# Performance work log

Hardware: AMD Instinct MI355X
Metric: run time of the kernel (lower is better)

The kernel has to match this reference:

```python
import jax, jax.numpy as jnp
import numpy as np

DIM = 1024
HEADS = 16
DIM_HEAD = 64
INNER = HEADS * DIM_HEAD  # 1024
SCALE = DIM_HEAD ** -0.5


def layernorm(x, gamma, beta, eps=1e-5):
    mu = jnp.mean(x, axis=-1, keepdims=True)
    var = jnp.var(x, axis=-1, keepdims=True)
    return (x - mu) * jax.lax.rsqrt(var + eps) * gamma + beta


def setup_inputs() -> dict:
    key = jax.random.key(0)
    ks = jax.random.split(key, 6)
    x = jax.random.normal(ks[0], (2, 2048, DIM), dtype=jnp.float32)
    # params (stored [in, out]; torch Linear does x @ W.T with W [out, in])
    w_q = jax.random.normal(ks[1], (DIM, INNER), dtype=jnp.float32) * (DIM ** -0.5)
    w_kv = jax.random.normal(ks[2], (DIM, 2 * INNER), dtype=jnp.float32) * (DIM ** -0.5)
    w_out = jax.random.normal(ks[3], (INNER, DIM), dtype=jnp.float32) * (INNER ** -0.5)
    b_out = jnp.zeros((DIM,), dtype=jnp.float32)
    gamma = jnp.ones((DIM,), dtype=jnp.float32)
    beta = jnp.zeros((DIM,), dtype=jnp.float32)
    return {"x": x, "w_q": w_q, "w_kv": w_kv, "w_out": w_out, "b_out": b_out,
            "gamma": gamma, "beta": beta}


def reference(x, w_q, w_kv, w_out, b_out, gamma, beta):
    b, n, _ = x.shape
    xn = layernorm(x, gamma, beta)
    q = xn @ w_q                           # [b, n, inner]
    kv = xn @ w_kv                         # [b, n, 2*inner]
    k, v = jnp.split(kv, 2, axis=-1)
    def split_heads(t):
        return t.reshape(b, n, HEADS, DIM_HEAD).transpose(0, 2, 1, 3)  # b h n d
    q, k, v = split_heads(q), split_heads(k), split_heads(v)
    dots = jnp.einsum('bhid,bhjd->bhij', q, k) * SCALE   # [b, h, n, n]
    attn = jax.nn.softmax(dots, axis=-1)
    out = jnp.einsum('bhij,bhjd->bhid', attn, v)          # [b, h, n, d]
    out = out.transpose(0, 2, 1, 3).reshape(b, n, INNER)  # b n (h d)
    return out @ w_out + b_out
```

## Files before the change

kernel.cpp:

```cpp
#include <hip/hip_runtime.h>

typedef unsigned short u16;
typedef u16   u16x8 __attribute__((ext_vector_type(8)));
typedef __bf16 bf16x8 __attribute__((ext_vector_type(8)));
typedef float f32x4 __attribute__((ext_vector_type(4)));
typedef float f32x2 __attribute__((ext_vector_type(2)));
typedef _Float16 f16x4 __attribute__((ext_vector_type(4)));
typedef _Float16 f16x8 __attribute__((ext_vector_type(8)));
typedef unsigned u32x2 __attribute__((ext_vector_type(2)));

__device__ __forceinline__ u16 f2b(float f){ __bf16 h=(__bf16)f; return __builtin_bit_cast(u16,h); }

__device__ __forceinline__ f32x4 mfma16(u16x8 a, u16x8 b, f32x4 c){
  return __builtin_amdgcn_mfma_f32_16x16x32_bf16(
      __builtin_bit_cast(bf16x8,a), __builtin_bit_cast(bf16x8,b), c, 0,0,0);
}

__device__ __forceinline__ void gl2lds16(const u16* g, u16* l){
  __builtin_amdgcn_global_load_lds((const __attribute__((address_space(1))) void*)g,
                                   (__attribute__((address_space(3))) void*)l, 16, 0, 0);
}

__global__ __launch_bounds__(256) void ln_kernel(const float* __restrict__ x,
                                                 const float* __restrict__ gamma,
                                                 const float* __restrict__ beta,
                                                 u16* __restrict__ xn){
  const int row = blockIdx.x, t = threadIdx.x;
  const float4 v = ((const float4*)(x + (size_t)row*1024))[t];
  float s  = v.x+v.y+v.z+v.w;
  float sq = v.x*v.x+v.y*v.y+v.z*v.z+v.w*v.w;
  for (int m=1;m<64;m<<=1){ s += __shfl_xor(s,m); sq += __shfl_xor(sq,m); }
  __shared__ float red[8];
  const int w=t>>6, l=t&63;
  if(l==0){ red[w]=s; red[4+w]=sq; }
  __syncthreads();
  const float S  = red[0]+red[1]+red[2]+red[3];
  const float SQ = red[4]+red[5]+red[6]+red[7];
  const float mu = S*(1.f/1024.f);
  const float var= SQ*(1.f/1024.f)-mu*mu;
  const float rs = rsqrtf(var+1e-5f);
  const float4 g4=((const float4*)gamma)[t], b4=((const float4*)beta)[t];
  u16 o0=f2b((v.x-mu)*rs*g4.x+b4.x);
  u16 o1=f2b((v.y-mu)*rs*g4.y+b4.y);
  u16 o2=f2b((v.z-mu)*rs*g4.z+b4.z);
  u16 o3=f2b((v.w-mu)*rs*g4.w+b4.w);
  uint2 p; p.x=(unsigned)o0|((unsigned)o1<<16); p.y=(unsigned)o2|((unsigned)o3<<16);
  ((uint2*)(xn + (size_t)row*1024))[t]=p;
}

__global__ __launch_bounds__(256) void wtrans_all_kernel(const float* __restrict__ wq,
    const float* __restrict__ wkv, const float* __restrict__ wout,
    u16* __restrict__ wqkvt, u16* __restrict__ woutt){
  __shared__ float tile[64][65];
  const int bx=blockIdx.x, t=threadIdx.x;
  const float* in; u16* out; int C, cxx;
  if(bx<16){ in=wq;  out=wqkvt;           C=1024; cxx=bx; }
  else if(bx<48){ in=wkv; out=wqkvt+1024*1024; C=2048; cxx=bx-16; }
  else { in=wout; out=woutt;             C=1024; cxx=bx-48; }
  const int R=1024;
  const int c0=cxx*64, r0=blockIdx.y*64;
  {
    const int r=t>>2, cc=t&3;
    const float* gp = in + (size_t)(r0+r)*C + c0 + cc*16;
    #pragma unroll
    for(int i=0;i<4;i++){
      float4 f=((const float4*)gp)[i];
      tile[r][cc*16+i*4+0]=f.x; tile[r][cc*16+i*4+1]=f.y;
      tile[r][cc*16+i*4+2]=f.z; tile[r][cc*16+i*4+3]=f.w;
    }
  }
  __syncthreads();
  const int c=t>>2, rc=t&3;
  u16x8 a,b;
  #pragma unroll
  for(int i=0;i<8;i++) a[i]=f2b(tile[rc*16+i][c]);
  #pragma unroll
  for(int i=0;i<8;i++) b[i]=f2b(tile[rc*16+8+i][c]);
  u16* op = out + (size_t)(c0+c)*R + r0 + rc*16;
  *(u16x8*)op=a; *(u16x8*)(op+8)=b;
}

template<int MODE,int TM>
__global__ __launch_bounds__(256) void gemm_bt_kernel(const u16* __restrict__ A,
    const u16* __restrict__ Bt, u16* __restrict__ outQ, u16* __restrict__ outK,
    u16* __restrict__ outV, float* __restrict__ outF, const float* __restrict__ bias,
    float scale, int M, int N, int K){
  constexpr int MT = TM/32;
  __shared__ u16 As[TM*64];
  __shared__ u16 Bs[128*64];
  const int t=threadIdx.x, w=t>>6, l=t&63, qd=l>>4, ln=l&15;
  const int m0=blockIdx.y*TM, n0=blockIdx.x*128;
  const int wm=(w>>1)*(TM/2), wn=(w&1)*64;
  f32x4 acc[MT][4] = {};
  const int nK = K>>6;
  for(int kt=0; kt<nK; kt++){
    const int k0=kt*64;
    #pragma unroll
    for(int p=0;p<MT;p++){
      const int cid=p*256+t, r=cid>>3, pc=cid&7, g=pc^(r&7);
      gl2lds16(A + (size_t)(m0+r)*K + k0 + g*8, &As[(p*256 + (t&192))*8]);
    }
    #pragma unroll
    for(int p=0;p<4;p++){
      const int cid=p*256+t, r=cid>>3, pc=cid&7, g=pc^(r&7);
      gl2lds16(Bt + (size_t)(n0+r)*K + k0 + g*8, &Bs[(p*256 + (t&192))*8]);
    }
    __syncthreads();
    #pragma unroll
    for(int ks=0;ks<2;ks++){
      u16x8 af[MT], bf[4];
      #pragma unroll
      for(int mt=0;mt<MT;mt++){
        const int m=wm+mt*16+ln, kc=ks*4+qd, pcc=kc^(m&7);
        af[mt]=*(const u16x8*)&As[m*64 + pcc*8];
      }
      #pragma unroll
      for(int nt=0;nt<4;nt++){
        const int n=wn+nt*16+ln, kc=ks*4+qd, pcc=kc^(n&7);
        bf[nt]=*(const u16x8*)&Bs[n*64 + pcc*8];
      }
      #pragma unroll
      for(int mt=0;mt<MT;mt++)
        #pragma unroll
        for(int nt=0;nt<4;nt++)
          acc[mt][nt]=mfma16(af[mt],bf[nt],acc[mt][nt]);
    }
    __syncthreads();
  }
  if(MODE==1){
    #pragma unroll
    for(int mt=0;mt<MT;mt++)
      #pragma unroll
      for(int rr=0;rr<4;rr++){
        const int row = m0+wm+mt*16+qd*4+rr;
        #pragma unroll
        for(int nt=0;nt<4;nt++){
          const int col = n0+wn+nt*16+ln;
          outF[(size_t)row*N+col]=acc[mt][nt][rr]+bias[col];
        }
      }
  } else if(n0<1024){
    #pragma unroll
    for(int mt=0;mt<MT;mt++)
      #pragma unroll
      for(int rr=0;rr<4;rr++){
        const int row = m0+wm+mt*16+qd*4+rr;
        #pragma unroll
        for(int nt=0;nt<4;nt++)
          outQ[(size_t)row*1024 + n0+wn+nt*16+ln]=f2b(acc[mt][nt][rr]*scale);
      }
  } else if(n0<2048){
    u16* kp = outK + (size_t)((m0>>11)*16 + ((n0-1024+wn)>>6))*131072;
    const int jb = (m0&2047) + wm;
    #pragma unroll
    for(int mt=0;mt<MT;mt++)
      #pragma unroll
      for(int rr=0;rr<4;rr++){
        const int j = jb + mt*16 + qd*4 + rr;
        #pragma unroll
        for(int nt=0;nt<4;nt++)
          kp[(size_t)j*64 + nt*16+ln]=f2b(acc[mt][nt][rr]);
      }
  } else {
    u16* vpp = outV + (size_t)((m0>>11)*16 + ((n0-2048+wn)>>6))*131072;
    const int jb = (m0&2047) + wm;
    #pragma unroll
    for(int mt=0;mt<MT;mt++){
      const int j = jb + mt*16 + qd*4;
      const int vbase = ((j>>5)*4 + ((j>>2)&3))*512 + ((j>>4)&1)*4;
      #pragma unroll
      for(int nt=0;nt<4;nt++){
        const auto lo=__builtin_amdgcn_cvt_pkrtz(acc[mt][nt][0],acc[mt][nt][1]);
        const auto hi=__builtin_amdgcn_cvt_pkrtz(acc[mt][nt][2],acc[mt][nt][3]);
        uint2 w2; w2.x=__builtin_bit_cast(unsigned,lo); w2.y=__builtin_bit_cast(unsigned,hi);
        *(uint2*)&vpp[vbase + (nt*16+ln)*8] = w2;
      }
    }
  }
}

__global__ __launch_bounds__(256,4) void attn_kernel(const u16* __restrict__ Q,
    const u16* __restrict__ Kp, const u16* __restrict__ Vp, u16* __restrict__ O){
  __shared__ u16 Ks[8192];
  __shared__ u16 Vs[8192];
  const int qt=blockIdx.x, h=blockIdx.y, bb=blockIdx.z;
  const int t=threadIdx.x, w=t>>6, l=t&63, qd=l>>4, ln=l&15;
  const int q0=qt*64;
  const size_t baseQ=(size_t)bb*2048*1024 + h*64;
  const size_t baseKV=(size_t)(bb*16+h)*131072;
  u16x8 qf[2];
  #pragma unroll
  for(int ks=0;ks<2;ks++)
    qf[ks] = *(const u16x8*)(Q + baseQ + (size_t)(q0+w*16+ln)*1024 + ks*32+qd*8);
  f32x2 l2={0.f,0.f};
  f32x4 o_acc[4]={};
  const f32x4 zf={0.f,0.f,0.f,0.f};

  for(int j0=0;j0<2048;j0+=128){
    __syncthreads();
    #pragma unroll
    for(int p=0;p<4;p++){
      const int r=(p*256+t)>>3, g=(t&7)^((t>>3)&7);
      gl2lds16(Kp + baseKV + (size_t)(j0+r)*64 + g*8, &Ks[(p*256+(t&192))*8]);
    }
    #pragma unroll
    for(int p=0;p<4;p++){
      gl2lds16(Vp + baseKV + (size_t)(j0>>5)*2048 + (size_t)(p*256+t)*8,
               &Vs[(p*256+(t&192))*8]);
    }
    __syncthreads();

    #pragma unroll
    for(int jh=0;jh<2;jh++){
      f32x4 s[4];
      #pragma unroll
      for(int ks=0;ks<2;ks++){
        u16x8 kf[4];
        #pragma unroll
        for(int j4=0;j4<4;j4++){
          const int row=(jh*4+j4)*16+ln;
          kf[j4]=*(const u16x8*)&Ks[row*64 + (((ks*4+qd)^(ln&7))*8)];
        }
        #pragma unroll
        for(int j4=0;j4<4;j4++)
          s[j4] = ks? mfma16(kf[j4],qf[1],s[j4]) : mfma16(kf[j4],qf[0],zf);
      }
      #pragma unroll
      for(int al=0;al<2;al++){
        const int a=jh*2+al;
        f16x8 vf2[4];
        #pragma unroll
        for(int dt=0;dt<4;dt++)
          vf2[dt]=*(const f16x8*)&Vs[((a*4+qd)*64 + dt*16+ln)*8];
        #pragma unroll
        for(int tt=0;tt<2;tt++){
          const int j4l=al*2+tt;
          const float p0=exp2f(s[j4l][0]), p1=exp2f(s[j4l][1]);
          const float p2=exp2f(s[j4l][2]), p3=exp2f(s[j4l][3]);
          f32x2 pa; pa.x=p0; pa.y=p1;
          f32x2 pb; pb.x=p2; pb.y=p3;
          l2+=pa+pb;
          const auto lo=__builtin_amdgcn_cvt_pkrtz(p0,p1);
          const auto hi=__builtin_amdgcn_cvt_pkrtz(p2,p3);
          u32x2 pu; pu.x=__builtin_bit_cast(unsigned,lo); pu.y=__builtin_bit_cast(unsigned,hi);
          const f16x4 pf=__builtin_bit_cast(f16x4,pu);
          #pragma unroll
          for(int dt=0;dt<4;dt++){
            const f16x4 vf=tt? __builtin_shufflevector(vf2[dt],vf2[dt],4,5,6,7)
                             : __builtin_shufflevector(vf2[dt],vf2[dt],0,1,2,3);
            o_acc[dt]=__builtin_amdgcn_mfma_f32_16x16x16f16(pf,vf,o_acc[dt],0,0,0);
          }
        }
      }
    }
  }

  float li=l2.x+l2.y;
  li+=__shfl_xor(li,16);
  li+=__shfl_xor(li,32);
  const float linv=1.f/li;
  #pragma unroll
  for(int rr=0;rr<4;rr++){
    const float lr=__shfl(linv,qd*4+rr);
    const int row=q0+w*16+qd*4+rr;
    #pragma unroll
    for(int dt=0;dt<4;dt++)
      O[baseQ + (size_t)row*1024 + dt*16+ln]=f2b(o_acc[dt][rr]*lr);
  }
}

extern "C" void kernel_launch(void* const* d_in, const int* in_sizes, int n_in,
                              void* d_out, int out_size, void* d_ws, size_t ws_size,
                              hipStream_t stream) {
  const float* x     = (const float*)d_in[0];
  const float* w_q   = (const float*)d_in[1];
  const float* w_kv  = (const float*)d_in[2];
  const float* w_out = (const float*)d_in[3];
  const float* b_out = (const float*)d_in[4];
  const float* gamma = (const float*)d_in[5];
  const float* beta  = (const float*)d_in[6];
  float* out = (float*)d_out;

  char* ws=(char*)d_ws;
  size_t off=0;
  u16* xn    =(u16*)(ws+off); off += (size_t)4096*1024*2;
  u16* wqkvt =(u16*)(ws+off); off += (size_t)3072*1024*2;
  u16* woutt =(u16*)(ws+off); off += (size_t)1024*1024*2;
  u16* qb    =(u16*)(ws+off); off += (size_t)4096*1024*2;
  u16* kpb   =(u16*)(ws+off); off += (size_t)4096*1024*2;
  u16* vpb   =(u16*)(ws+off); off += (size_t)4096*1024*2;
  u16* ob    =(u16*)(ws+off); off += (size_t)4096*1024*2;

  ln_kernel<<<4096,256,0,stream>>>(x,gamma,beta,xn);
  wtrans_all_kernel<<<dim3(64,16),256,0,stream>>>(w_q,w_kv,w_out,wqkvt,woutt);

  const float SCALE_Q = 0.125f*1.4426950408889634f;
  gemm_bt_kernel<2,128><<<dim3(24,32),256,0,stream>>>(xn,wqkvt,qb,kpb,vpb,nullptr,nullptr,SCALE_Q,4096,3072,1024);
  attn_kernel<<<dim3(32,16,2),256,0,stream>>>(qb,kpb,vpb,ob);
  gemm_bt_kernel<1,64><<<dim3(8,64),256,0,stream>>>(ob,woutt,nullptr,nullptr,nullptr,out,b_out,1.f,4096,1024,1024);
}
```

Before: 199.4 us.

## Double-buffer K/V tiles in attention with 512-thread blocks and MFMA priority

The attention kernel now uses 512-thread blocks covering 128 query rows, halving the grid so each K/V tile loaded into LDS is shared by twice as many waves. K/V staging is double-buffered: the next tile is issued asynchronously while the current one is consumed, with a single barrier per iteration. MFMA sections are wrapped in s_setprio raises to favour matrix issue across waves. This doubles LDS use per block (64 KB) and may reduce occupancy. The 512-thread/4-blocks launch bound may also raise register pressure.

After: 198.0 us. Within noise of the previous version (-0.7%).

```diff
diff --git a/kernel.cpp b/kernel.cpp
--- a/kernel.cpp
+++ b/kernel.cpp
@@ -179,13 +179,13 @@
   }
 }
 
-__global__ __launch_bounds__(256,4) void attn_kernel(const u16* __restrict__ Q,
+__global__ __launch_bounds__(512,4) void attn_kernel(const u16* __restrict__ Q,
     const u16* __restrict__ Kp, const u16* __restrict__ Vp, u16* __restrict__ O){
-  __shared__ u16 Ks[8192];
-  __shared__ u16 Vs[8192];
+  __shared__ u16 Ks[2][8192];
+  __shared__ u16 Vs[2][8192];
   const int qt=blockIdx.x, h=blockIdx.y, bb=blockIdx.z;
   const int t=threadIdx.x, w=t>>6, l=t&63, qd=l>>4, ln=l&15;
-  const int q0=qt*64;
+  const int q0=qt*128;
   const size_t baseQ=(size_t)bb*2048*1024 + h*64;
   const size_t baseKV=(size_t)(bb*16+h)*131072;
   u16x8 qf[2];
@@ -196,20 +196,25 @@
   f32x4 o_acc[4]={};
   const f32x4 zf={0.f,0.f,0.f,0.f};
 
-  for(int j0=0;j0<2048;j0+=128){
-    __syncthreads();
-    #pragma unroll
-    for(int p=0;p<4;p++){
-      const int r=(p*256+t)>>3, g=(t&7)^((t>>3)&7);
-      gl2lds16(Kp + baseKV + (size_t)(j0+r)*64 + g*8, &Ks[(p*256+(t&192))*8]);
-    }
-    #pragma unroll
-    for(int p=0;p<4;p++){
-      gl2lds16(Vp + baseKV + (size_t)(j0>>5)*2048 + (size_t)(p*256+t)*8,
-               &Vs[(p*256+(t&192))*8]);
-    }
-    __syncthreads();
-
+  auto stage=[&](int buf,int j0){
+    #pragma unroll
+    for(int p=0;p<2;p++){
+      const int cid=p*512+t, r=cid>>3, g=(t&7)^((t>>3)&7);
+      gl2lds16(Kp + baseKV + (size_t)(j0+r)*64 + g*8, &Ks[buf][(p*512+(t&448))*8]);
+    }
+    #pragma unroll
+    for(int p=0;p<2;p++)
+      gl2lds16(Vp + baseKV + (size_t)(j0>>5)*2048 + (size_t)(p*512+t)*8,
+               &Vs[buf][(p*512+(t&448))*8]);
+  };
+
+  stage(0,0);
+  __syncthreads();
+  int cur=0;
+  for(int jt=0;jt<16;jt++){
+    if(jt<15) stage(cur^1,(jt+1)*128);
+    const u16* Kb=&Ks[cur][0];
+    const u16* Vb=&Vs[cur][0];
     #pragma unroll
     for(int jh=0;jh<2;jh++){
       f32x4 s[4];
@@ -219,11 +224,13 @@
         #pragma unroll
         for(int j4=0;j4<4;j4++){
           const int row=(jh*4+j4)*16+ln;
-          kf[j4]=*(const u16x8*)&Ks[row*64 + (((ks*4+qd)^(ln&7))*8)];
+          kf[j4]=*(const u16x8*)&Kb[row*64 + (((ks*4+qd)^(ln&7))*8)];
         }
+        __builtin_amdgcn_s_setprio(1);
         #pragma unroll
         for(int j4=0;j4<4;j4++)
           s[j4] = ks? mfma16(kf[j4],qf[1],s[j4]) : mfma16(kf[j4],qf[0],zf);
+        __builtin_amdgcn_s_setprio(0);
       }
       #pragma unroll
       for(int al=0;al<2;al++){
@@ -231,7 +238,7 @@
         f16x8 vf2[4];
         #pragma unroll
         for(int dt=0;dt<4;dt++)
-          vf2[dt]=*(const f16x8*)&Vs[((a*4+qd)*64 + dt*16+ln)*8];
+          vf2[dt]=*(const f16x8*)&Vb[((a*4+qd)*64 + dt*16+ln)*8];
         #pragma unroll
         for(int tt=0;tt<2;tt++){
           const int j4l=al*2+tt;
@@ -244,15 +251,19 @@
           const auto hi=__builtin_amdgcn_cvt_pkrtz(p2,p3);
           u32x2 pu; pu.x=__builtin_bit_cast(unsigned,lo); pu.y=__builtin_bit_cast(unsigned,hi);
           const f16x4 pf=__builtin_bit_cast(f16x4,pu);
+          __builtin_amdgcn_s_setprio(1);
           #pragma unroll
           for(int dt=0;dt<4;dt++){
             const f16x4 vf=tt? __builtin_shufflevector(vf2[dt],vf2[dt],4,5,6,7)
                              : __builtin_shufflevector(vf2[dt],vf2[dt],0,1,2,3);
             o_acc[dt]=__builtin_amdgcn_mfma_f32_16x16x16f16(pf,vf,o_acc[dt],0,0,0);
           }
+          __builtin_amdgcn_s_setprio(0);
         }
       }
     }
+    __syncthreads();
+    cur^=1;
   }
 
   float li=l2.x+l2.y;
@@ -296,6 +307,6 @@
 
   const float SCALE_Q = 0.125f*1.4426950408889634f;
   gemm_bt_kernel<2,128><<<dim3(24,32),256,0,stream>>>(xn,wqkvt,qb,kpb,vpb,nullptr,nullptr,SCALE_Q,4096,3072,1024);
-  attn_kernel<<<dim3(32,16,2),256,0,stream>>>(qb,kpb,vpb,ob);
+  attn_kernel<<<dim3(16,16,2),512,0,stream>>>(qb,kpb,vpb,ob);
   gemm_bt_kernel<1,64><<<dim3(8,64),256,0,stream>>>(ob,woutt,nullptr,nullptr,nullptr,out,b_out,1.f,4096,1024,1024);
 }
```
